# Performance work log

Hardware: AMD Instinct MI355X
Metric: run time of the kernel (lower is better)

## Reference

```python
import jax, jax.numpy as jnp
import numpy as np

B, T, D = 4, 1024, 1024
H, DH = 16, 64
FFN = 4096
CAPACITY = 0.25
C_VAR = 1.0
BETA_CE = 1.0
BETA_CU = 1.0
EPS = 1e-6


def _rmsnorm(x, w, eps=EPS):
    v = jnp.mean(jnp.square(x), axis=-1, keepdims=True)
    return x * jax.lax.rsqrt(v + eps) * w


def _rope(x, pos):
    # x: [B, S, H, DH], pos: [B, S] float positions
    half = x.shape[-1] // 2
    inv = 1.0 / (10000.0 ** (jnp.arange(half, dtype=jnp.float32) / half))
    ang = pos[:, :, None] * inv                      # [B, S, half]
    cos = jnp.cos(ang)[:, :, None, :]                # [B, S, 1, half]
    sin = jnp.sin(ang)[:, :, None, :]
    x1, x2 = x[..., :half], x[..., half:]
    return jnp.concatenate([x1 * cos - x2 * sin, x2 * cos + x1 * sin], axis=-1)


def _decoder(x, pos, ln1, wq, wk, wv, wo, ln2, wg, wu, wd):
    # Qwen2-style decoder layer: RMSNorm -> rotary causal MHA -> res -> RMSNorm -> SwiGLU -> res
    b, s, d = x.shape
    h = _rmsnorm(x, ln1)
    q = _rope((h @ wq).reshape(b, s, H, DH), pos)
    k = _rope((h @ wk).reshape(b, s, H, DH), pos)
    v = (h @ wv).reshape(b, s, H, DH)
    scores = jnp.einsum('bqhd,bkhd->bhqk', q, k) / jnp.sqrt(jnp.float32(DH))
    causal = jnp.tril(jnp.ones((s, s), dtype=bool))
    scores = jnp.where(causal, scores, jnp.finfo(scores.dtype).min)
    attn = jax.nn.softmax(scores, axis=-1)
    o = jnp.einsum('bhqk,bkhd->bqhd', attn, v).reshape(b, s, d) @ wo
    x = x + o
    h2 = _rmsnorm(x, ln2)
    return x + (jax.nn.silu(h2 @ wg) * (h2 @ wu)) @ wd


def _forward(hidden_states, ln1_1, wq1, wk1, wv1, wo1, ln2_1, wg1, wu1, wd1,
             ln1_2, wq2, wk2, wv2, wo2, ln2_2, wg2, wu2, wd2,
             prior_norm_w, prior_w):
    b, t, d = hidden_states.shape
    pos = jnp.broadcast_to(jnp.arange(t, dtype=jnp.float32)[None, :], (b, t))
    # decision layer: full-sequence decoder block
    processed = _decoder(hidden_states, pos, ln1_1, wq1, wk1, wv1, wo1, ln2_1, wg1, wu1, wd1)
    res = processed - hidden_states                  # actual_residual
    # prior network: RMSNorm + linear -> (mu_q, log_var_q)
    prior_h = _rmsnorm(hidden_states, prior_norm_w)
    mu_logvar = prior_h @ prior_w                    # [B, T, 2D]
    mu, logvar = mu_logvar[..., :d], mu_logvar[..., d:]
    # surprise router signals
    d_st = jnp.mean(jnp.square(res), axis=-1)        # [B, T]
    d_ch = jnp.mean(0.5 * (logvar - jnp.log(C_VAR)
                           + (C_VAR + jnp.square(res - mu)) * jnp.exp(-logvar) - 1.0), axis=-1)
    g = jax.nn.sigmoid(BETA_CE * (d_st - jnp.mean(d_st)) + BETA_CU * (d_ch - jnp.mean(d_ch)))
    # top-k selection, sorted by token index (as in the torch code)
    k_sel = max(1, int(t * CAPACITY))
    scores, idx = jax.lax.top_k(g, k_sel)            # [B, k]
    order = jnp.argsort(idx, axis=-1)
    idx = jnp.take_along_axis(idx, order, axis=-1)
    scores = jnp.take_along_axis(scores, order, axis=-1)
    # gather -> decoder layer on selected tokens -> soft-gated scatter back
    bidx = jnp.arange(b)[:, None]
    sel = processed[bidx, idx]                       # [B, k, D]
    y = _decoder(sel, idx.astype(jnp.float32), ln1_2, wq2, wk2, wv2, wo2, ln2_2, wg2, wu2, wd2)
    upd = sel + scores[..., None] * (y - sel)        # soft gating of the block residual
    return processed.at[bidx, idx].set(upd)


def setup_inputs():
    key = jax.random.key(0)
    ks = jax.random.split(key, 16)
    s = 0.02

    def w(k, shape):
        return jax.random.normal(k, shape, dtype=jnp.float32) * s

    inp = {'hidden_states': jax.random.normal(ks[0], (B, T, D), dtype=jnp.float32)}
    for i, n in enumerate(['wq1', 'wk1', 'wv1', 'wo1', 'wq2', 'wk2', 'wv2', 'wo2']):
        inp[n] = w(ks[1 + i], (D, D))
    inp['wg1'] = w(ks[9], (D, FFN)); inp['wu1'] = w(ks[10], (D, FFN)); inp['wd1'] = w(ks[11], (FFN, D))
    inp['wg2'] = w(ks[12], (D, FFN)); inp['wu2'] = w(ks[13], (D, FFN)); inp['wd2'] = w(ks[14], (FFN, D))
    for n in ['ln1_1', 'ln2_1', 'ln1_2', 'ln2_2', 'prior_norm_w']:
        inp[n] = jnp.ones((D,), dtype=jnp.float32)
    inp['prior_w'] = w(ks[15], (D, 2 * D))
    return inp


def reference(hidden_states, ln1_1, wq1, wk1, wv1, wo1, ln2_1, wg1, wu1, wd1,
              ln1_2, wq2, wk2, wv2, wo2, ln2_2, wg2, wu2, wd2,
              prior_norm_w, prior_w):
    return _forward(hidden_states, ln1_1, wq1, wk1, wv1, wo1, ln2_1, wg1, wu1, wd1,
                    ln1_2, wq2, wk2, wv2, wo2, ln2_2, wg2, wu2, wd2,
                    prior_norm_w, prior_w)
```

## Files before the change

### kernel.cpp

```cpp
#include <hip/hip_runtime.h>
#include <math.h>

#define Bdim 4
#define Tdim 1024
#define Ddim 1024
#define Hdim 16
#define DHdim 64
#define FFNdim 4096
#define KSEL 256
#define EPSf 1e-6f

typedef __attribute__((ext_vector_type(8))) short bf16x8;
typedef __attribute__((ext_vector_type(4))) float f32x4;
typedef __attribute__((ext_vector_type(4))) unsigned int u32x4;
typedef unsigned short ushort_t;

#define MFMA_BF16(a,b,c) __builtin_amdgcn_mfma_f32_16x16x32_bf16(a,b,c,0,0,0)

__device__ __forceinline__ int clamp_row(int r){ return r < 0 ? 0 : (r > Tdim-1 ? Tdim-1 : r); }

__device__ __forceinline__ void split8(const float* xs, u32x4* hi, u32x4* lo){
  unsigned int hm[8], lm[8];
  #pragma unroll
  for (int i=0;i<8;i++){
    unsigned int b = __float_as_uint(xs[i]);
    hm[i] = b & 0xFFFF0000u;
    lm[i] = __float_as_uint(xs[i] - __uint_as_float(hm[i]));
  }
  u32x4 h, l;
  #pragma unroll
  for (int i=0;i<4;i++){
    h[i] = (hm[2*i] >> 16) | hm[2*i+1];
    l[i] = (lm[2*i] >> 16) | (lm[2*i+1] & 0xFFFF0000u);
  }
  *hi = h; *lo = l;
}

__device__ __forceinline__ void split1(float x, unsigned int* h16, unsigned int* l16){
  unsigned int b = __float_as_uint(x);
  unsigned int hm = b & 0xFFFF0000u;
  *h16 = hm >> 16;
  *l16 = __float_as_uint(x - __uint_as_float(hm)) >> 16;
}

__global__ void k_fallback(const float* __restrict__ in, float* __restrict__ out, int n){
  int i = blockIdx.x*blockDim.x + threadIdx.x;
  if (i < n) out[i] = in[i];
}

__global__ void k_init_sel(int* __restrict__ selidx, float* __restrict__ selsc, int n){
  int i = blockIdx.x*blockDim.x + threadIdx.x;
  if (i < n){ selidx[i] = i & (KSEL-1); selsc[i] = 0.f; }
}

__global__ __launch_bounds__(256) void k_rmsnorm(const float* __restrict__ x, const float* __restrict__ w,
                          float* __restrict__ y){
  int tok = blockIdx.x;
  const float* xp = x + (size_t)tok*Ddim;
  float* yp = y + (size_t)tok*Ddim;
  int tid = threadIdx.x;
  float s = 0.f;
  float xv[4];
  #pragma unroll
  for (int u = 0; u < 4; u++){ xv[u] = xp[tid + 256*u]; s += xv[u]*xv[u]; }
  __shared__ float red[256];
  red[tid]=s; __syncthreads();
  for (int st=128; st>0; st>>=1){ if (tid<st) red[tid]+=red[tid+st]; __syncthreads(); }
  float r = 1.0f/sqrtf(red[0]/(float)Ddim + EPSf);
  #pragma unroll
  for (int u = 0; u < 4; u++) yp[tid + 256*u] = xv[u]*r*w[tid + 256*u];
}

__global__ __launch_bounds__(256) void k_rmsnorm_sp(const float* __restrict__ x, const float* __restrict__ w,
                          ushort_t* __restrict__ yh, ushort_t* __restrict__ yl){
  int tok = blockIdx.x;
  const float* xp = x + (size_t)tok*Ddim;
  size_t ybase = (size_t)tok*Ddim;
  int tid = threadIdx.x;
  float s = 0.f;
  float xv[4];
  #pragma unroll
  for (int u = 0; u < 4; u++){ xv[u] = xp[tid + 256*u]; s += xv[u]*xv[u]; }
  __shared__ float red[256];
  red[tid]=s; __syncthreads();
  for (int st=128; st>0; st>>=1){ if (tid<st) red[tid]+=red[tid+st]; __syncthreads(); }
  float r = 1.0f/sqrtf(red[0]/(float)Ddim + EPSf);
  #pragma unroll
  for (int u = 0; u < 4; u++){
    float yv = xv[u]*r*w[tid + 256*u];
    unsigned int h16,l16; split1(yv,&h16,&l16);
    yh[ybase + tid + 256*u] = (ushort_t)h16;
    yl[ybase + tid + 256*u] = (ushort_t)l16;
  }
}

__global__ void k_rope(float* __restrict__ x, const int* __restrict__ posidx, int S, int n){
  int e = blockIdx.x*blockDim.x + threadIdx.x;
  if (e >= n) return;
  int j = e & 31;
  int q = e >> 9;
  int t = q % S;
  float pos = posidx ? (float)clamp_row(posidx[q]) : (float)t;
  float inv = exp2f(-0.4152410118609203f * (float)j);
  float ang = pos * inv;
  float c = cosf(ang), s = sinf(ang);
  size_t base = ((size_t)(e >> 5)) * 64;
  float x1 = x[base + j], x2 = x[base + 32 + j];
  x[base + j]      = x1*c - x2*s;
  x[base + 32 + j] = x2*c + x1*s;
}

__global__ void k_rope_sp(const float* __restrict__ x, const int* __restrict__ posidx, int S, int n,
                          ushort_t* __restrict__ Xh, ushort_t* __restrict__ Xl){
  int e = blockIdx.x*blockDim.x + threadIdx.x;
  if (e >= n) return;
  int j = e & 31;
  int q = e >> 9;
  int t = q % S;
  float pos = posidx ? (float)clamp_row(posidx[q]) : (float)t;
  float inv = exp2f(-0.4152410118609203f * (float)j);
  float ang = pos * inv;
  float c = cosf(ang), s = sinf(ang);
  size_t base = ((size_t)(e >> 5)) * 64;
  float x1 = x[base + j], x2 = x[base + 32 + j];
  float y1 = x1*c - x2*s;
  float y2 = x2*c + x1*s;
  unsigned int h16,l16;
  split1(y1,&h16,&l16); Xh[base + j] = (ushort_t)h16; Xl[base + j] = (ushort_t)l16;
  split1(y2,&h16,&l16); Xh[base + 32 + j] = (ushort_t)h16; Xl[base + 32 + j] = (ushort_t)l16;
}

__global__ __launch_bounds__(256) void k_split_w(const float* __restrict__ W,
                          ushort_t* __restrict__ Wh, ushort_t* __restrict__ Wl, int K, int N){
  __shared__ float fs[64][65];
  int n0 = blockIdx.x*64, k0 = blockIdx.y*64;
  int tid = threadIdx.x;
  #pragma unroll
  for (int i=0;i<16;i++){
    int idx = tid + 256*i;
    int r = idx >> 6, c = idx & 63;
    fs[r][c] = W[(size_t)(k0 + r)*N + n0 + c];
  }
  __syncthreads();
  int n = tid >> 2, kq = tid & 3;
  unsigned int hw[8], lw[8];
  #pragma unroll
  for (int i=0;i<16;i+=2){
    float v0 = fs[kq*16+i][n], v1 = fs[kq*16+i+1][n];
    unsigned int h0,l0,h1,l1;
    split1(v0,&h0,&l0); split1(v1,&h1,&l1);
    hw[i>>1] = h0 | (h1<<16);
    lw[i>>1] = l0 | (l1<<16);
  }
  size_t base = (size_t)(n0+n)*K + k0 + kq*16;
  u32x4 a = {hw[0],hw[1],hw[2],hw[3]};
  u32x4 b = {hw[4],hw[5],hw[6],hw[7]};
  *(u32x4*)&Wh[base] = a;
  *(u32x4*)&Wh[base+8] = b;
  u32x4 c2 = {lw[0],lw[1],lw[2],lw[3]};
  u32x4 d2 = {lw[4],lw[5],lw[6],lw[7]};
  *(u32x4*)&Wl[base] = c2;
  *(u32x4*)&Wl[base+8] = d2;
}

__global__ __launch_bounds__(256) void k_attn_mfma(const float* __restrict__ q, const float* __restrict__ k,
                       const float* __restrict__ v, float* __restrict__ o, int S){
  __shared__ ushort_t Kh[64*64], Kl[64*64];
  __shared__ ushort_t Vh[64*64], Vl[64*64];
  __shared__ float Pds[4*16*68];
  const int qt = blockIdx.x, h = blockIdx.y, b = blockIdx.z;
  const int q0 = qt*64;
  const int tid = threadIdx.x;
  const int lane = tid & 63;
  const int ln15 = lane & 15, lk = lane >> 4;
  const int wv = tid >> 6;
  const int qbase = wv*16;
  bf16x8 qa_h[2], qa_l[2];
  {
    const float* qp = q + (((size_t)b*S + q0 + qbase + ln15)*Hdim + h)*64 + lk*8;
    #pragma unroll
    for (int ks=0; ks<2; ks++){
      float xs[8];
      #pragma unroll
      for (int i=0;i<8;i++) xs[i] = qp[ks*32 + i];
      u32x4 hi, lo; split8(xs, &hi, &lo);
      qa_h[ks] = *(bf16x8*)&hi;
      qa_l[ks] = *(bf16x8*)&lo;
    }
  }
  float m_i[4], l_i[4];
  f32x4 oacc[4];
  #pragma unroll
  for (int r=0;r<4;r++){ m_i[r] = -3.4e38f; l_i[r] = 0.f; }
  #pragma unroll
  for (int fd=0;fd<4;fd++){ f32x4 z = {0.f,0.f,0.f,0.f}; oacc[fd] = z; }
  float* Pw = Pds + wv*(16*68);
  for (int j0 = 0; j0 <= q0; j0 += 64){
    __syncthreads();
    {
      int row = tid >> 2;
      int s0 = (tid & 3)*2;
      const float* kp = k + (((size_t)b*S + j0 + row)*Hdim + h)*64 + s0*8;
      #pragma unroll
      for (int g=0; g<2; g++){
        int slot = s0 + g;
        float xs[8];
        #pragma unroll
        for (int i=0;i<8;i++) xs[i] = kp[g*8 + i];
        u32x4 hi, lo; split8(xs, &hi, &lo);
        int base = row*64 + ((slot ^ (row&7))*8);
        *(u32x4*)&Kh[base] = hi;
        *(u32x4*)&Kl[base] = lo;
      }
    }
    {
      int j = tid & 31;
      int dbase = (tid >> 5)*8;
      const float* vp0 = v + (((size_t)b*S + j0 + 2*j)*Hdim + h)*64 + dbase;
      const float* vp1 = vp0 + (size_t)Hdim*64;
      float x0[8], x1[8];
      #pragma unroll
      for (int i=0;i<8;i++){ x0[i]=vp0[i]; x1[i]=vp1[i]; }
      unsigned int* VhW = (unsigned int*)Vh;
      unsigned int* VlW = (unsigned int*)Vl;
      #pragma unroll
      for (int i=0;i<8;i++){
        int d = dbase + i;
        unsigned int h0,l0,h1,l1;
        split1(x0[i], &h0, &l0); split1(x1[i], &h1, &l1);
        int off = d*32 + (((j>>2) ^ (d&7))*4) + (j&3);
        VhW[off] = h0 | (h1<<16);
        VlW[off] = l0 | (l1<<16);
      }
    }
    __syncthreads();
    f32x4 sacc[4];
    #pragma unroll
    for (int fj=0;fj<4;fj++){ f32x4 z = {0.f,0.f,0.f,0.f}; sacc[fj] = z; }
    #pragma unroll
    for (int ks=0; ks<2; ks++){
      #pragma unroll
      for (int fj=0;fj<4;fj++){
        int kr = fj*16 + ln15;
        int idx = kr*64 + (((ks*4+lk) ^ (kr&7))*8);
        bf16x8 kb_h = *(const bf16x8*)&Kh[idx];
        bf16x8 kb_l = *(const bf16x8*)&Kl[idx];
        sacc[fj] = MFMA_BF16(qa_h[ks], kb_h, sacc[fj]);
        sacc[fj] = MFMA_BF16(qa_h[ks], kb_l, sacc[fj]);
        sacc[fj] = MFMA_BF16(qa_l[ks], kb_h, sacc[fj]);
      }
    }
    #pragma unroll
    for (int fj=0;fj<4;fj++){
      int key = j0 + fj*16 + ln15;
      #pragma unroll
      for (int r=0;r<4;r++){
        float sv = sacc[fj][r]*0.125f;
        int qrow = q0 + qbase + lk*4 + r;
        sacc[fj][r] = (key > qrow) ? -3.4e38f : sv;
      }
    }
    float p[4][4];
    #pragma unroll
    for (int r=0;r<4;r++){
      float mt = fmaxf(fmaxf(sacc[0][r],sacc[1][r]), fmaxf(sacc[2][r],sacc[3][r]));
      #pragma unroll
      for (int off=1; off<16; off<<=1) mt = fmaxf(mt, __shfl_xor(mt, off));
      float m_new = fmaxf(m_i[r], mt);
      float alpha = expf(m_i[r] - m_new);
      float rs = 0.f;
      #pragma unroll
      for (int fj=0;fj<4;fj++){
        p[fj][r] = expf(sacc[fj][r] - m_new);
        rs += p[fj][r];
      }
      #pragma unroll
      for (int off=1; off<16; off<<=1) rs += __shfl_xor(rs, off);
      l_i[r] = l_i[r]*alpha + rs;
      m_i[r] = m_new;
      #pragma unroll
      for (int fd=0;fd<4;fd++) oacc[fd][r] *= alpha;
    }
    #pragma unroll
    for (int fj=0;fj<4;fj++)
      #pragma unroll
      for (int r=0;r<4;r++)
        Pw[(lk*4+r)*68 + fj*16 + ln15] = p[fj][r];
    #pragma unroll
    for (int ks=0; ks<2; ks++){
      f32x4 pf0 = *(const f32x4*)&Pw[ln15*68 + ks*32 + lk*8];
      f32x4 pf1 = *(const f32x4*)&Pw[ln15*68 + ks*32 + lk*8 + 4];
      float xs[8] = {pf0[0],pf0[1],pf0[2],pf0[3],pf1[0],pf1[1],pf1[2],pf1[3]};
      u32x4 hi, lo; split8(xs, &hi, &lo);
      bf16x8 pa_h = *(bf16x8*)&hi;
      bf16x8 pa_l = *(bf16x8*)&lo;
      #pragma unroll
      for (int fd=0;fd<4;fd++){
        int d = fd*16 + ln15;
        int idx = d*64 + (((ks*4+lk) ^ (d&7))*8);
        bf16x8 vb_h = *(const bf16x8*)&Vh[idx];
        bf16x8 vb_l = *(const bf16x8*)&Vl[idx];
        oacc[fd] = MFMA_BF16(pa_h, vb_h, oacc[fd]);
        oacc[fd] = MFMA_BF16(pa_h, vb_l, oacc[fd]);
        oacc[fd] = MFMA_BF16(pa_l, vb_h, oacc[fd]);
      }
    }
  }
  #pragma unroll
  for (int r=0;r<4;r++){
    float inv_l = 1.0f/l_i[r];
    #pragma unroll
    for (int fd=0;fd<4;fd++){
      o[(((size_t)b*S + q0 + qbase + lk*4 + r)*Hdim + h)*64 + fd*16 + ln15] = oacc[fd][r]*inv_l;
    }
  }
}

__global__ __launch_bounds__(256) void k_attn_ps(
    const ushort_t* __restrict__ Qph, const ushort_t* __restrict__ Qpl,
    const ushort_t* __restrict__ Kph, const ushort_t* __restrict__ Kpl,
    const ushort_t* __restrict__ Vph, const ushort_t* __restrict__ Vpl,
    ushort_t* __restrict__ Oh, ushort_t* __restrict__ Ol, int S){
  __shared__ ushort_t Kh[64*64], Kl[64*64];
  __shared__ ushort_t Vh[64*64], Vl[64*64];
  __shared__ float Pds[4*16*68];
  const int qt = blockIdx.x, h = blockIdx.y, b = blockIdx.z;
  const int q0 = qt*64;
  const int tid = threadIdx.x;
  const int lane = tid & 63;
  const int ln15 = lane & 15, lk = lane >> 4;
  const int wv = tid >> 6;
  const int qbase = wv*16;
  bf16x8 qa_h[2], qa_l[2];
  {
    size_t qoff = (((size_t)b*S + q0 + qbase + ln15)*Hdim + h)*64;
    #pragma unroll
    for (int ks=0; ks<2; ks++){
      qa_h[ks] = *(const bf16x8*)&Qph[qoff + ks*32 + lk*8];
      qa_l[ks] = *(const bf16x8*)&Qpl[qoff + ks*32 + lk*8];
    }
  }
  float m_i[4], lp[4];
  f32x4 oacc[4];
  #pragma unroll
  for (int r=0;r<4;r++){ m_i[r] = -3.4e38f; lp[r] = 0.f; }
  #pragma unroll
  for (int fd=0;fd<4;fd++){ f32x4 z = {0.f,0.f,0.f,0.f}; oacc[fd] = z; }
  float* Pw = Pds + wv*(16*68);
  for (int j0 = 0; j0 <= q0; j0 += 64){
    __syncthreads();
    #pragma unroll
    for (int g=0; g<2; g++){
      int row = g*32 + (tid >> 3);
      int ks = tid & 7;
      size_t ga = (((size_t)b*S + j0 + row)*Hdim + h)*64 + ks*8;
      u32x4 hi = *(const u32x4*)&Kph[ga];
      u32x4 lo = *(const u32x4*)&Kpl[ga];
      int base = row*64 + ((ks ^ (row&7))*8);
      *(u32x4*)&Kh[base] = hi;
      *(u32x4*)&Kl[base] = lo;
    }
    {
      int j = tid & 31;
      int dbase = (tid >> 5)*8;
      size_t g0 = (((size_t)b*S + j0 + 2*j)*Hdim + h)*64 + dbase;
      size_t g1 = g0 + (size_t)Hdim*64;
      u32x4 ah = *(const u32x4*)&Vph[g0];
      u32x4 bh = *(const u32x4*)&Vph[g1];
      u32x4 al = *(const u32x4*)&Vpl[g0];
      u32x4 bl = *(const u32x4*)&Vpl[g1];
      unsigned int* VhW = (unsigned int*)Vh;
      unsigned int* VlW = (unsigned int*)Vl;
      #pragma unroll
      for (int i=0;i<4;i++){
        int d0 = dbase + 2*i, d1 = d0 + 1;
        int off0 = d0*32 + (((j>>2) ^ (d0&7))*4) + (j&3);
        int off1 = d1*32 + (((j>>2) ^ (d1&7))*4) + (j&3);
        VhW[off0] = (ah[i] & 0xFFFFu) | (bh[i] << 16);
        VhW[off1] = (ah[i] >> 16)     | (bh[i] & 0xFFFF0000u);
        VlW[off0] = (al[i] & 0xFFFFu) | (bl[i] << 16);
        VlW[off1] = (al[i] >> 16)     | (bl[i] & 0xFFFF0000u);
      }
    }
    __syncthreads();
    f32x4 sacc[4];
    #pragma unroll
    for (int fj=0;fj<4;fj++){ f32x4 z = {0.f,0.f,0.f,0.f}; sacc[fj] = z; }
    #pragma unroll
    for (int ks=0; ks<2; ks++){
      #pragma unroll
      for (int fj=0;fj<4;fj++){
        int kr = fj*16 + ln15;
        int idx = kr*64 + (((ks*4+lk) ^ (kr&7))*8);
        bf16x8 kb_h = *(const bf16x8*)&Kh[idx];
        bf16x8 kb_l = *(const bf16x8*)&Kl[idx];
        sacc[fj] = MFMA_BF16(qa_h[ks], kb_h, sacc[fj]);
        sacc[fj] = MFMA_BF16(qa_h[ks], kb_l, sacc[fj]);
        sacc[fj] = MFMA_BF16(qa_l[ks], kb_h, sacc[fj]);
      }
    }
    #pragma unroll
    for (int fj=0;fj<4;fj++){
      int key = j0 + fj*16 + ln15;
      #pragma unroll
      for (int r=0;r<4;r++){
        float sv = sacc[fj][r]*0.125f;
        int qrow = q0 + qbase + lk*4 + r;
        sacc[fj][r] = (key > qrow) ? -3.4e38f : sv;
      }
    }
    float tm[4];
    #pragma unroll
    for (int r=0;r<4;r++)
      tm[r] = fmaxf(fmaxf(sacc[0][r],sacc[1][r]), fmaxf(sacc[2][r],sacc[3][r]));
    bool okl = (tm[0] <= m_i[0]+8.f) & (tm[1] <= m_i[1]+8.f)
             & (tm[2] <= m_i[2]+8.f) & (tm[3] <= m_i[3]+8.f);
    float p[4][4];
    if (__all(okl)){
      #pragma unroll
      for (int r=0;r<4;r++){
        #pragma unroll
        for (int fj=0;fj<4;fj++){
          float pv = expf(sacc[fj][r] - m_i[r]);
          p[fj][r] = pv;
          lp[r] += pv;
        }
      }
    } else {
      #pragma unroll
      for (int r=0;r<4;r++){
        float mt = tm[r];
        #pragma unroll
        for (int off=1; off<16; off<<=1) mt = fmaxf(mt, __shfl_xor(mt, off));
        float m_new = fmaxf(m_i[r], mt);
        float alpha = expf(m_i[r] - m_new);
        lp[r] *= alpha;
        #pragma unroll
        for (int fd=0;fd<4;fd++) oacc[fd][r] *= alpha;
        m_i[r] = m_new;
        #pragma unroll
        for (int fj=0;fj<4;fj++){
          float pv = expf(sacc[fj][r] - m_new);
          p[fj][r] = pv;
          lp[r] += pv;
        }
      }
    }
    #pragma unroll
    for (int fj=0;fj<4;fj++)
      #pragma unroll
      for (int r=0;r<4;r++)
        Pw[(lk*4+r)*68 + fj*16 + ln15] = p[fj][r];
    #pragma unroll
    for (int ks=0; ks<2; ks++){
      f32x4 pf0 = *(const f32x4*)&Pw[ln15*68 + ks*32 + lk*8];
      f32x4 pf1 = *(const f32x4*)&Pw[ln15*68 + ks*32 + lk*8 + 4];
      float xs[8] = {pf0[0],pf0[1],pf0[2],pf0[3],pf1[0],pf1[1],pf1[2],pf1[3]};
      u32x4 hi, lo; split8(xs, &hi, &lo);
      bf16x8 pa_h = *(bf16x8*)&hi;
      bf16x8 pa_l = *(bf16x8*)&lo;
      #pragma unroll
      for (int fd=0;fd<4;fd++){
        int d = fd*16 + ln15;
        int idx = d*64 + (((ks*4+lk) ^ (d&7))*8);
        bf16x8 vb_h = *(const bf16x8*)&Vh[idx];
        bf16x8 vb_l = *(const bf16x8*)&Vl[idx];
        oacc[fd] = MFMA_BF16(pa_h, vb_h, oacc[fd]);
        oacc[fd] = MFMA_BF16(pa_h, vb_l, oacc[fd]);
        oacc[fd] = MFMA_BF16(pa_l, vb_h, oacc[fd]);
      }
    }
  }
  #pragma unroll
  for (int r=0;r<4;r++){
    float l = lp[r];
    #pragma unroll
    for (int off=1; off<16; off<<=1) l += __shfl_xor(l, off);
    float inv_l = 1.0f/l;
    #pragma unroll
    for (int fd=0;fd<4;fd++){
      float val = oacc[fd][r]*inv_l;
      unsigned int h16,l16; split1(val,&h16,&l16);
      size_t cix = (((size_t)b*S + q0 + qbase + lk*4 + r)*Hdim + h)*64 + fd*16 + ln15;
      Oh[cix] = (ushort_t)h16;
      Ol[cix] = (ushort_t)l16;
    }
  }
}

__global__ __launch_bounds__(256) void k_gemm_mfma(
    const float* __restrict__ A, const float* __restrict__ W,
    float* __restrict__ C, const float* __restrict__ addv,
    int K, int ldw, int ldc){
  __shared__ ushort_t Ah[128*32], Al[128*32], Bh[128*32], Bl[128*32];
  const int tid = threadIdx.x;
  const int row0 = blockIdx.y*128, col0 = blockIdx.x*128;
  const int lane = tid & 63;
  const int ln15 = lane & 15, lk = lane >> 4;
  const int wv = tid >> 6;
  const int wrow0 = (wv >> 1)*64, wcol0 = (wv & 1)*64;
  const int arow = tid >> 2;
  const int aks  = tid & 3;
  const int bcol = tid & 127;
  const int bks0 = tid >> 7;
  f32x4 acc[4][4];
  #pragma unroll
  for (int i=0;i<4;i++)
    #pragma unroll
    for (int j=0;j<4;j++){ f32x4 z = {0.f,0.f,0.f,0.f}; acc[i][j] = z; }
  for (int k0 = 0; k0 < K; k0 += 32){
    #pragma unroll
    for (int g=0; g<2; g++){
      int row = g*64 + arow;
      const float* ap = A + (size_t)(row0+row)*K + k0 + aks*8;
      float xs[8];
      #pragma unroll
      for (int i=0;i<8;i++) xs[i] = ap[i];
      u32x4 hi, lo; split8(xs, &hi, &lo);
      int base = row*32 + ((aks ^ ((row>>1)&3))*8);
      *(u32x4*)&Ah[base] = hi;
      *(u32x4*)&Al[base] = lo;
    }
    #pragma unroll
    for (int g=0; g<2; g++){
      int ks = bks0 + 2*g;
      const float* wp = W + (size_t)(k0 + ks*8)*ldw + col0 + bcol;
      float xs[8];
      #pragma unroll
      for (int i=0;i<8;i++) xs[i] = wp[(size_t)i*ldw];
      u32x4 hi, lo; split8(xs, &hi, &lo);
      int base = bcol*32 + ((ks ^ ((bcol>>1)&3))*8);
      *(u32x4*)&Bh[base] = hi;
      *(u32x4*)&Bl[base] = lo;
    }
    __syncthreads();
    bf16x8 ah[4], al[4];
    #pragma unroll
    for (int fi=0;fi<4;fi++){
      int r = wrow0 + fi*16 + ln15;
      int idx = r*32 + ((lk ^ ((r>>1)&3))*8);
      ah[fi] = *(const bf16x8*)&Ah[idx];
      al[fi] = *(const bf16x8*)&Al[idx];
    }
    #pragma unroll
    for (int fj=0;fj<4;fj++){
      int c = wcol0 + fj*16 + ln15;
      int idx = c*32 + ((lk ^ ((c>>1)&3))*8);
      bf16x8 bh = *(const bf16x8*)&Bh[idx];
      bf16x8 bl = *(const bf16x8*)&Bl[idx];
      #pragma unroll
      for (int fi=0;fi<4;fi++){
        acc[fi][fj] = MFMA_BF16(ah[fi], bh, acc[fi][fj]);
        acc[fi][fj] = MFMA_BF16(ah[fi], bl, acc[fi][fj]);
        acc[fi][fj] = MFMA_BF16(al[fi], bh, acc[fi][fj]);
      }
    }
    __syncthreads();
  }
  #pragma unroll
  for (int fi=0;fi<4;fi++){
    #pragma unroll
    for (int fj=0;fj<4;fj++){
      f32x4 v = acc[fi][fj];
      int cc = col0 + wcol0 + fj*16 + ln15;
      #pragma unroll
      for (int r=0;r<4;r++){
        size_t cix = (size_t)(row0 + wrow0 + fi*16 + lk*4 + r)*ldc + cc;
        float val = v[r];
        if (addv) val += addv[cix];
        C[cix] = val;
      }
    }
  }
}

__global__ __launch_bounds__(512) void k_gemm_ps(
    const ushort_t* __restrict__ Ahp, const ushort_t* __restrict__ Alp, int lda,
    const ushort_t* __restrict__ Bhp, const ushort_t* __restrict__ Blp, int ldb,
    float* __restrict__ C, ushort_t* __restrict__ Chp, ushort_t* __restrict__ Clp,
    const float* __restrict__ addv, int K, int ldc){
  __shared__ ushort_t Ah[128*32], Al[128*32], Bh[128*32], Bl[128*32];
  const int tid = threadIdx.x;
  const int row0 = blockIdx.y*128, col0 = blockIdx.x*128;
  const int lane = tid & 63;
  const int ln15 = lane & 15, lk = lane >> 4;
  const int wv = tid >> 6;
  const int wrow0 = (wv >> 2)*64, wcol0 = (wv & 3)*32;
  const int t8 = tid >> 2, ks4 = tid & 3;
  const int sbase = t8*32 + ((ks4 ^ ((t8>>1)&3))*8);
  const size_t gaBase = (size_t)(row0 + t8)*lda + ks4*8;
  const size_t gbBase = (size_t)(col0 + t8)*ldb + ks4*8;

  f32x4 acc[4][2];
  #pragma unroll
  for (int i=0;i<4;i++)
    #pragma unroll
    for (int j=0;j<2;j++){ f32x4 z = {0.f,0.f,0.f,0.f}; acc[i][j] = z; }

  u32x4 rAh = *(const u32x4*)&Ahp[gaBase];
  u32x4 rAl = *(const u32x4*)&Alp[gaBase];
  u32x4 rBh = *(const u32x4*)&Bhp[gbBase];
  u32x4 rBl = *(const u32x4*)&Blp[gbBase];

  for (int k0 = 0; k0 < K; k0 += 32){
    __syncthreads();
    *(u32x4*)&Ah[sbase] = rAh;
    *(u32x4*)&Al[sbase] = rAl;
    *(u32x4*)&Bh[sbase] = rBh;
    *(u32x4*)&Bl[sbase] = rBl;
    __syncthreads();
    if (k0 + 32 < K){
      rAh = *(const u32x4*)&Ahp[gaBase + k0 + 32];
      rAl = *(const u32x4*)&Alp[gaBase + k0 + 32];
      rBh = *(const u32x4*)&Bhp[gbBase + k0 + 32];
      rBl = *(const u32x4*)&Blp[gbBase + k0 + 32];
    }
    bf16x8 ah[4], al[4];
    #pragma unroll
    for (int fi=0;fi<4;fi++){
      int r = wrow0 + fi*16 + ln15;
      int idx = r*32 + ((lk ^ ((r>>1)&3))*8);
      ah[fi] = *(const bf16x8*)&Ah[idx];
      al[fi] = *(const bf16x8*)&Al[idx];
    }
    #pragma unroll
// ... 370 lines not shown
  const float* xp = x0 + (size_t)tok*Ddim;
  const float* mu = muB + (size_t)tok*Ddim;
  const float* lv = lvB + (size_t)tok*Ddim;
  float s1=0.f, s2=0.f;
  for (int i=tid;i<Ddim;i+=256){
    float r = pp[i]-xp[i];
    s1 += r*r;
    float t = r - mu[i];
    float l = lv[i];
    s2 += 0.5f*(l + (1.0f + t*t)*expf(-l) - 1.0f);
  }
  __shared__ float red[256], red2[256];
  red[tid]=s1; red2[tid]=s2; __syncthreads();
  for (int st=128; st>0; st>>=1){ if (tid<st){red[tid]+=red[tid+st]; red2[tid]+=red2[tid+st];} __syncthreads(); }
  if (tid==0){ dst[tok]=red[0]/(float)Ddim; dch[tok]=red2[0]/(float)Ddim; }
}

__global__ __launch_bounds__(1024) void k_gate(const float* __restrict__ dst, const float* __restrict__ dch,
                        float* __restrict__ g){
  int tid = threadIdx.x;
  float s1=0.f, s2=0.f;
  for (int i=tid; i<Bdim*Tdim; i+=1024){ s1+=dst[i]; s2+=dch[i]; }
  __shared__ float r1[1024], r2[1024];
  r1[tid]=s1; r2[tid]=s2; __syncthreads();
  for (int st=512; st>0; st>>=1){ if(tid<st){r1[tid]+=r1[tid+st]; r2[tid]+=r2[tid+st];} __syncthreads(); }
  float m1 = r1[0]/(float)(Bdim*Tdim), m2 = r2[0]/(float)(Bdim*Tdim);
  for (int i=tid; i<Bdim*Tdim; i+=1024){
    float z = (dst[i]-m1) + (dch[i]-m2);
    g[i] = 1.0f/(1.0f+expf(-z));
  }
}

__global__ __launch_bounds__(1024) void k_select(const float* __restrict__ g, int* __restrict__ selidx,
                         float* __restrict__ selsc){
  int b = blockIdx.x, t = threadIdx.x;
  __shared__ float gs[1024];
  __shared__ int flag[1024];
  float gv = g[b*Tdim + t];
  if (!(gv == gv)) gv = -3.4e38f;
  gs[t] = gv; __syncthreads();
  float gi = gs[t];
  int rank = 0;
  for (int j=0;j<Tdim;j++){
    float gj = gs[j];
    rank += (gj > gi) || (gj == gi && j < t);
  }
  int sel = (rank < KSEL) ? 1 : 0;
  flag[t] = sel; __syncthreads();
  if (sel){
    int pos = 0;
    for (int j=0;j<t;j++) pos += flag[j];
    if (pos < KSEL){
      selidx[b*KSEL+pos] = t;
      selsc[b*KSEL+pos] = gi;
    }
  }
}

__global__ __launch_bounds__(256) void k_gather(const float* __restrict__ proc, const int* __restrict__ selidx,
                         float* __restrict__ sel){
  int j = blockIdx.x, b = blockIdx.y, tid = threadIdx.x;
  int row = clamp_row(selidx[b*KSEL+j]);
  const float* src = proc + ((size_t)b*Tdim + row)*Ddim;
  float* dst = sel + ((size_t)b*KSEL + j)*Ddim;
  for (int d=tid; d<Ddim; d+=256) dst[d]=src[d];
}

__global__ void k_out(const float* __restrict__ proc, float* __restrict__ out, int n){
  int i = blockIdx.x*blockDim.x + threadIdx.x;
  if (i<n) out[i] = proc[i];
}

__global__ __launch_bounds__(256) void k_scatter(const float* __restrict__ sel, const float* __restrict__ y,
                          const float* __restrict__ selsc, const int* __restrict__ selidx,
                          float* __restrict__ out){
  int j = blockIdx.x, b = blockIdx.y, tid = threadIdx.x;
  int row = clamp_row(selidx[b*KSEL+j]);
  float s = selsc[b*KSEL+j];
  const float* sp = sel + ((size_t)b*KSEL + j)*Ddim;
  const float* yp = y + ((size_t)b*KSEL + j)*Ddim;
  float* op = out + ((size_t)b*Tdim + row)*Ddim;
  for (int d=tid; d<Ddim; d+=256){
    op[d] = sp[d] + s*(yp[d]-sp[d]);
  }
}

extern "C" void kernel_launch(void* const* d_in, const int* in_sizes, int n_in,
                              void* d_out, int out_size, void* d_ws, size_t ws_size,
                              hipStream_t stream){
  (void)in_sizes; (void)n_in; (void)out_size;
  const float* hidden = (const float*)d_in[0];
  const float* wq1 = (const float*)d_in[1];
  const float* wk1 = (const float*)d_in[2];
  const float* wv1 = (const float*)d_in[3];
  const float* wo1 = (const float*)d_in[4];
  const float* wq2 = (const float*)d_in[5];
  const float* wk2 = (const float*)d_in[6];
  const float* wv2 = (const float*)d_in[7];
  const float* wo2 = (const float*)d_in[8];
  const float* wg1 = (const float*)d_in[9];
  const float* wu1 = (const float*)d_in[10];
  const float* wd1 = (const float*)d_in[11];
  const float* wg2 = (const float*)d_in[12];
  const float* wu2 = (const float*)d_in[13];
  const float* wd2 = (const float*)d_in[14];
  const float* ln1_1 = (const float*)d_in[15];
  const float* ln2_1 = (const float*)d_in[16];
  const float* ln1_2 = (const float*)d_in[17];
  const float* ln2_2 = (const float*)d_in[18];
  const float* prior_norm = (const float*)d_in[19];
  const float* prior_w = (const float*)d_in[20];

  const size_t A = (size_t)Bdim*Tdim*Ddim;
  const size_t Q = (size_t)Bdim*KSEL*Ddim;
  const int n = (int)A;
  const int MT = Bdim*Tdim;
  const int M2 = Bdim*KSEL;

  const size_t WELEMS = 34u*1024*1024;
  size_t need_old = (4*A + 16384) * sizeof(float);
  size_t need_new = need_old + 2*WELEMS*sizeof(ushort_t);

  if (ws_size < need_old){
    k_fallback<<<(n+255)/256,256,0,stream>>>(hidden, (float*)d_out, n);
    return;
  }

  float* ws = (float*)d_ws;
  float* R0 = ws;
  float* R1 = ws + 1*A;
  float* R2 = ws + 2*A;
  float* R3 = ws + 3*A;
  float* dstb = ws + 4*A;
  float* dchb = dstb + 4096;
  float* gb   = dchb + 4096;
  float* selsc= gb + 4096;
  int*   selidx = (int*)(selsc + 1024);

  k_init_sel<<<4,256,0,stream>>>(selidx, selsc, Bdim*KSEL);

  if (ws_size >= need_new){
    ushort_t* wpb = (ushort_t*)(ws + 4*A + 16384);
    size_t cur = 0;
    const size_t M1x1 = (size_t)1024*1024;
    const size_t M1x4 = (size_t)1024*4096;
    #define ALLOCW(nm, KN) ushort_t* nm##_h = wpb + cur; ushort_t* nm##_l = wpb + cur + (KN); cur += 2*(size_t)(KN);
    ALLOCW(pwq1, M1x1) ALLOCW(pwk1, M1x1) ALLOCW(pwv1, M1x1) ALLOCW(pwo1, M1x1)
    ALLOCW(pwq2, M1x1) ALLOCW(pwk2, M1x1) ALLOCW(pwv2, M1x1) ALLOCW(pwo2, M1x1)
    ALLOCW(pwg1, M1x4) ALLOCW(pwu1, M1x4) ALLOCW(pwd1, M1x4)
    ALLOCW(pwg2, M1x4) ALLOCW(pwu2, M1x4) ALLOCW(pwd2, M1x4)
    ALLOCW(ppw, (size_t)2048*1024)
    #undef ALLOCW

    k_split_w<<<dim3(16,16),256,0,stream>>>(wq1, pwq1_h, pwq1_l, 1024, 1024);
    k_split_w<<<dim3(16,16),256,0,stream>>>(wk1, pwk1_h, pwk1_l, 1024, 1024);
    k_split_w<<<dim3(16,16),256,0,stream>>>(wv1, pwv1_h, pwv1_l, 1024, 1024);
    k_split_w<<<dim3(16,16),256,0,stream>>>(wo1, pwo1_h, pwo1_l, 1024, 1024);
    k_split_w<<<dim3(16,16),256,0,stream>>>(wq2, pwq2_h, pwq2_l, 1024, 1024);
    k_split_w<<<dim3(16,16),256,0,stream>>>(wk2, pwk2_h, pwk2_l, 1024, 1024);
    k_split_w<<<dim3(16,16),256,0,stream>>>(wv2, pwv2_h, pwv2_l, 1024, 1024);
    k_split_w<<<dim3(16,16),256,0,stream>>>(wo2, pwo2_h, pwo2_l, 1024, 1024);
    k_split_w<<<dim3(64,16),256,0,stream>>>(wg1, pwg1_h, pwg1_l, 1024, 4096);
    k_split_w<<<dim3(64,16),256,0,stream>>>(wu1, pwu1_h, pwu1_l, 1024, 4096);
    k_split_w<<<dim3(16,64),256,0,stream>>>(wd1, pwd1_h, pwd1_l, 4096, 1024);
    k_split_w<<<dim3(64,16),256,0,stream>>>(wg2, pwg2_h, pwg2_l, 1024, 4096);
    k_split_w<<<dim3(64,16),256,0,stream>>>(wu2, pwu2_h, pwu2_l, 1024, 4096);
    k_split_w<<<dim3(16,64),256,0,stream>>>(wd2, pwd2_h, pwd2_l, 4096, 1024);
    k_split_w<<<dim3(32,16),256,0,stream>>>(prior_w, ppw_h, ppw_l, 1024, 2048);

    ushort_t* Hh = (ushort_t*)R0; ushort_t* Hl = Hh + A;
    k_rmsnorm_sp<<<MT,256,0,stream>>>(hidden, ln1_1, Hh, Hl);
    ushort_t* Vp_h = (ushort_t*)R3; ushort_t* Vp_l = Vp_h + A;
    k_gemm_qkv<<<dim3(8, MT/128, 3),512,0,stream>>>(Hh,Hl,1024,
        pwq1_h,pwq1_l, pwk1_h,pwk1_l, pwv1_h,pwv1_l, 1024,
        R1, R2, Vp_h, Vp_l, 1024, 1024);
    int nr = MT*Hdim*32;
    ushort_t* Qp_h = (ushort_t*)R0; ushort_t* Qp_l = Qp_h + A;
    k_rope_sp<<<(nr+255)/256,256,0,stream>>>(R1, nullptr, Tdim, nr, Qp_h, Qp_l);
    ushort_t* Kp_h = (ushort_t*)R1; ushort_t* Kp_l = Kp_h + A;
    k_rope_sp<<<(nr+255)/256,256,0,stream>>>(R2, nullptr, Tdim, nr, Kp_h, Kp_l);
    ushort_t* Op_h = (ushort_t*)R2; ushort_t* Op_l = Op_h + A;
    k_attn_ps<<<dim3(Tdim/64,Hdim,Bdim),256,0,stream>>>(Qp_h,Qp_l, Kp_h,Kp_l, Vp_h,Vp_l, Op_h,Op_l, Tdim);
    k_gemm_ps<<<dim3(8, MT/128),512,0,stream>>>(Op_h,Op_l,1024, pwo1_h,pwo1_l,1024, R1, nullptr,nullptr, hidden, 1024, 1024);
    ushort_t* H2h = (ushort_t*)R0; ushort_t* H2l = H2h + A;
    k_rmsnorm_sp<<<MT,256,0,stream>>>(R1, ln2_1, H2h, H2l);
    ushort_t* ACTh = (ushort_t*)R3; ushort_t* ACTl = ACTh + A;
    for (int c = 0; c < 4; c++){
      k_gemm_dual_ps<<<dim3(16, MT/128),512,0,stream>>>(H2h,H2l,1024,
          pwg1_h + (size_t)c*M1x1, pwg1_l + (size_t)c*M1x1,
          pwu1_h + (size_t)c*M1x1, pwu1_l + (size_t)c*M1x1, 1024,
          ACTh, ACTl, 1024, 1024);
      k_gemm_ps<<<dim3(8, MT/128),512,0,stream>>>(ACTh,ACTl,1024,
          pwd1_h + (size_t)c*1024, pwd1_l + (size_t)c*1024, 4096,
          R2, nullptr,nullptr, (c==0 ? R1 : R2), 1024, 1024);
    }

    ushort_t* PHh = (ushort_t*)R0; ushort_t* PHl = PHh + A;
    k_rmsnorm_sp<<<MT,256,0,stream>>>(hidden, prior_norm, PHh, PHl);
    k_gemm_qkv<<<dim3(8, MT/128, 2),512,0,stream>>>(PHh,PHl,1024,
        ppw_h,ppw_l, ppw_h + M1x1, ppw_l + M1x1, nullptr,nullptr, 1024,
        R1, R3, nullptr,nullptr, 1024, 1024);
    k_dstch2<<<MT,256,0,stream>>>(R2, hidden, R1, R3, dstb, dchb);
    k_gate<<<1,1024,0,stream>>>(dstb, dchb, gb);
    k_select<<<Bdim,1024,0,stream>>>(gb, selidx, selsc);
    float* SELX = R0;
    k_gather<<<dim3(KSEL,Bdim),256,0,stream>>>(R2, selidx, SELX);

    ushort_t* h2h = (ushort_t*)R1;        ushort_t* h2l = h2h + Q;
    k_rmsnorm_sp<<<M2,256,0,stream>>>(SELX, ln1_2, h2h, h2l);
    float* q2f = R1 + Q;
    float* k2f = R1 + 2*Q;
    ushort_t* v2h = (ushort_t*)(R1 + 3*Q); ushort_t* v2l = v2h + Q;
    k_gemm_qkv<<<dim3(8, M2/128, 3),512,0,stream>>>(h2h,h2l,1024,
        pwq2_h,pwq2_l, pwk2_h,pwk2_l, pwv2_h,pwv2_l, 1024,
        q2f, k2f, v2h, v2l, 1024, 1024);
    int nr2 = M2*Hdim*32;
    ushort_t* q2ph = (ushort_t*)(R0 + Q);   ushort_t* q2pl = q2ph + Q;
    ushort_t* k2ph = (ushort_t*)(R0 + 2*Q); ushort_t* k2pl = k2ph + Q;
    k_rope_sp<<<(nr2+255)/256,256,0,stream>>>(q2f, selidx, KSEL, nr2, q2ph, q2pl);
    k_rope_sp<<<(nr2+255)/256,256,0,stream>>>(k2f, selidx, KSEL, nr2, k2ph, k2pl);
    ushort_t* o2h = (ushort_t*)(R0 + 3*Q);  ushort_t* o2l = o2h + Q;
    k_attn_ps<<<dim3(KSEL/64,Hdim,Bdim),256,0,stream>>>(q2ph,q2pl, k2ph,k2pl, v2h,v2l, o2h,o2l, KSEL);
    float* X12 = R1 + Q;
    k_gemm_ps<<<dim3(8, M2/128),512,0,stream>>>(o2h,o2l,1024, pwo2_h,pwo2_l,1024, X12, nullptr,nullptr, SELX, 1024, 1024);
    ushort_t* h22h = (ushort_t*)(R1 + 2*Q); ushort_t* h22l = h22h + Q;
    k_rmsnorm_sp<<<M2,256,0,stream>>>(X12, ln2_2, h22h, h22l);
    ushort_t* act2h = (ushort_t*)(R1 + 3*Q); ushort_t* act2l = act2h + Q;
    float* Y = R3;
    for (int c = 0; c < 4; c++){
      k_gemm_dual_ps<<<dim3(16, M2/128),512,0,stream>>>(h22h,h22l,1024,
          pwg2_h + (size_t)c*M1x1, pwg2_l + (size_t)c*M1x1,
          pwu2_h + (size_t)c*M1x1, pwu2_l + (size_t)c*M1x1, 1024,
          act2h, act2l, 1024, 1024);
      k_gemm_ps<<<dim3(8, M2/128),512,0,stream>>>(act2h,act2l,1024,
          pwd2_h + (size_t)c*1024, pwd2_l + (size_t)c*1024, 4096,
          Y, nullptr,nullptr, (c==0 ? X12 : Y), 1024, 1024);
    }
    k_out<<<(n+255)/256,256,0,stream>>>(R2, (float*)d_out, n);
    k_scatter<<<dim3(KSEL,Bdim),256,0,stream>>>(SELX, Y, selsc, selidx, (float*)d_out);
    return;
  }

  k_rmsnorm<<<MT,256,0,stream>>>(hidden, ln1_1, R0);
  dim3 gD(Ddim/128, MT/128);
  k_gemm_mfma<<<gD,256,0,stream>>>(R0, wq1, R1, nullptr, Ddim, Ddim, Ddim);
  k_gemm_mfma<<<gD,256,0,stream>>>(R0, wk1, R2, nullptr, Ddim, Ddim, Ddim);
  k_gemm_mfma<<<gD,256,0,stream>>>(R0, wv1, R3, nullptr, Ddim, Ddim, Ddim);
  int nr = MT*Hdim*32;
  k_rope<<<(nr+255)/256,256,0,stream>>>(R1, nullptr, Tdim, nr);
  k_rope<<<(nr+255)/256,256,0,stream>>>(R2, nullptr, Tdim, nr);
  k_attn_mfma<<<dim3(Tdim/64,Hdim,Bdim),256,0,stream>>>(R1, R2, R3, R0, Tdim);
  k_gemm_mfma<<<gD,256,0,stream>>>(R0, wo1, R1, hidden, Ddim, Ddim, Ddim);
  k_rmsnorm<<<MT,256,0,stream>>>(R1, ln2_1, R2);
  for (int c = 0; c < 4; c++){
    k_gemm_dual_mfma<<<dim3(1024/64, MT/128),256,0,stream>>>(R2, wg1 + (size_t)c*1024, wu1 + (size_t)c*1024,
                                                  R3, Ddim, FFNdim, 1024);
    k_gemm_mfma<<<dim3(Ddim/128, MT/128),256,0,stream>>>(R3, wd1 + (size_t)c*1024*Ddim, R0,
                                             (c==0 ? R1 : R0), 1024, Ddim, Ddim);
  }
  k_rmsnorm<<<MT,256,0,stream>>>(hidden, prior_norm, R1);
  k_gemm_mfma<<<dim3(2*Ddim/128, MT/128),256,0,stream>>>(R1, prior_w, R2, nullptr, Ddim, 2*Ddim, 2*Ddim);
  k_dstch<<<MT,256,0,stream>>>(R0, hidden, R2, dstb, dchb);
  k_gate<<<1,1024,0,stream>>>(dstb, dchb, gb);
  k_select<<<Bdim,1024,0,stream>>>(gb, selidx, selsc);
  k_gather<<<dim3(KSEL,Bdim),256,0,stream>>>(R0, selidx, R1);
  k_rmsnorm<<<M2,256,0,stream>>>(R1, ln1_2, R2);
  dim3 gD2(Ddim/128, M2/128);
  k_gemm_mfma<<<gD2,256,0,stream>>>(R2, wq2, R2+Q,   nullptr, Ddim, Ddim, Ddim);
  k_gemm_mfma<<<gD2,256,0,stream>>>(R2, wk2, R2+2*Q, nullptr, Ddim, Ddim, Ddim);
  k_gemm_mfma<<<gD2,256,0,stream>>>(R2, wv2, R2+3*Q, nullptr, Ddim, Ddim, Ddim);
  int nr2 = M2*Hdim*32;
  k_rope<<<(nr2+255)/256,256,0,stream>>>(R2+Q,   nullptr, KSEL, nr2);
  k_rope<<<(nr2+255)/256,256,0,stream>>>(R2+2*Q, nullptr, KSEL, nr2);
  k_rope<<<(nr2+255)/256,256,0,stream>>>(R2+Q,   selidx, KSEL, 0);
  k_attn_mfma<<<dim3(KSEL/64,Hdim,Bdim),256,0,stream>>>(R2+Q, R2+2*Q, R2+3*Q, R3, KSEL);
  k_gemm_mfma<<<gD2,256,0,stream>>>(R3, wo2, R3+Q, R1, Ddim, Ddim, Ddim);
  k_rmsnorm<<<M2,256,0,stream>>>(R3+Q, ln2_2, R3+2*Q);
  for (int c = 0; c < 4; c++){
    k_gemm_dual_mfma<<<dim3(1024/64, M2/128),256,0,stream>>>(R3+2*Q, wg2 + (size_t)c*1024, wu2 + (size_t)c*1024,
                                                  R3+3*Q, Ddim, FFNdim, 1024);
    k_gemm_mfma<<<dim3(Ddim/128, M2/128),256,0,stream>>>(R3+3*Q, wd2 + (size_t)c*1024*Ddim, R2,
                                             (c==0 ? R3+Q : R2), 1024, Ddim, Ddim);
  }
  k_out<<<(n+255)/256,256,0,stream>>>(R0, (float*)d_out, n);
  k_scatter<<<dim3(KSEL,Bdim),256,0,stream>>>(R1, R2, selsc, selidx, (float*)d_out);
}
```

Measured before the change: 1.379 ms.

## Prefetch KV tiles in attention, batch weight splits, reverse tile order, fix rope positions

The causal attention kernel now loads the next K/V tile from global memory into registers while the current tile is being computed, so load latency overlaps with MFMA work. Query tiles are visited in reverse order so the longest causal blocks are scheduled first, which should balance the tail of the grid. The many per-weight hi/lo split launches are merged into three batched launches indexed by blockIdx.z, cutting launch overhead. The second-layer rope calls are changed to use the selected indices for both Q and K, which alters behaviour on that path. The prefetch costs extra registers per thread.

New measurement: 1.420 ms. 3.0% more time.

```diff
diff --git a/kernel.cpp b/kernel.cpp
--- a/kernel.cpp
+++ b/kernel.cpp
@@ -130,6 +130,46 @@
   split1(y2,&h16,&l16); Xh[base + 32 + j] = (ushort_t)h16; Xl[base + 32 + j] = (ushort_t)l16;
 }
 
+struct SplitJobs {
+  const float* W[8];
+  ushort_t* Wh[8];
+  ushort_t* Wl[8];
+};
+__global__ __launch_bounds__(256) void k_split_wz(SplitJobs jobs, int K, int N){
+  const float* W = jobs.W[blockIdx.z];
+  ushort_t* Wh = jobs.Wh[blockIdx.z];
+  ushort_t* Wl = jobs.Wl[blockIdx.z];
+  __shared__ float fs[64][65];
+  int n0 = blockIdx.x*64, k0 = blockIdx.y*64;
+  int tid = threadIdx.x;
+  #pragma unroll
+  for (int i=0;i<16;i++){
+    int idx = tid + 256*i;
+    int r = idx >> 6, c = idx & 63;
+    fs[r][c] = W[(size_t)(k0 + r)*N + n0 + c];
+  }
+  __syncthreads();
+  int n = tid >> 2, kq = tid & 3;
+  unsigned int hw[8], lw[8];
+  #pragma unroll
+  for (int i=0;i<16;i+=2){
+    float v0 = fs[kq*16+i][n], v1 = fs[kq*16+i+1][n];
+    unsigned int h0,l0,h1,l1;
+    split1(v0,&h0,&l0); split1(v1,&h1,&l1);
+    hw[i>>1] = h0 | (h1<<16);
+    lw[i>>1] = l0 | (l1<<16);
+  }
+  size_t base = (size_t)(n0+n)*K + k0 + kq*16;
+  u32x4 a = {hw[0],hw[1],hw[2],hw[3]};
+  u32x4 b = {hw[4],hw[5],hw[6],hw[7]};
+  *(u32x4*)&Wh[base] = a;
+  *(u32x4*)&Wh[base+8] = b;
+  u32x4 c2 = {lw[0],lw[1],lw[2],lw[3]};
+  u32x4 d2 = {lw[4],lw[5],lw[6],lw[7]};
+  *(u32x4*)&Wl[base] = c2;
+  *(u32x4*)&Wl[base+8] = d2;
+}
+
 __global__ __launch_bounds__(256) void k_split_w(const float* __restrict__ W,
                           ushort_t* __restrict__ Wh, ushort_t* __restrict__ Wl, int K, int N){
   __shared__ float fs[64][65];
@@ -324,7 +364,8 @@
   __shared__ ushort_t Kh[64*64], Kl[64*64];
   __shared__ ushort_t Vh[64*64], Vl[64*64];
   __shared__ float Pds[4*16*68];
-  const int qt = blockIdx.x, h = blockIdx.y, b = blockIdx.z;
+  const int qt = (gridDim.x - 1) - blockIdx.x;
+  const int h = blockIdx.y, b = blockIdx.z;
   const int q0 = qt*64;
   const int tid = threadIdx.x;
   const int lane = tid & 63;
@@ -340,6 +381,19 @@
       qa_l[ks] = *(const bf16x8*)&Qpl[qoff + ks*32 + lk*8];
     }
   }
+  const int krow = tid >> 3, kks = tid & 7;
+  const int vj = tid & 31, vdbase = (tid >> 5)*8;
+  u32x4 rKh[2], rKl[2], rVah, rVbh, rVal, rVbl;
+  #define LOAD_KV(J0) { \
+    size_t ga0 = (((size_t)b*S + (J0) + krow)*Hdim + h)*64 + kks*8; \
+    size_t ga1 = (((size_t)b*S + (J0) + 32 + krow)*Hdim + h)*64 + kks*8; \
+    rKh[0] = *(const u32x4*)&Kph[ga0]; rKl[0] = *(const u32x4*)&Kpl[ga0]; \
+    rKh[1] = *(const u32x4*)&Kph[ga1]; rKl[1] = *(const u32x4*)&Kpl[ga1]; \
+    size_t g0 = (((size_t)b*S + (J0) + 2*vj)*Hdim + h)*64 + vdbase; \
+    size_t g1 = g0 + (size_t)Hdim*64; \
+    rVah = *(const u32x4*)&Vph[g0]; rVbh = *(const u32x4*)&Vph[g1]; \
+    rVal = *(const u32x4*)&Vpl[g0]; rVbl = *(const u32x4*)&Vpl[g1]; }
+
   float m_i[4], lp[4];
   f32x4 oacc[4];
   #pragma unroll
@@ -347,42 +401,33 @@
   #pragma unroll
   for (int fd=0;fd<4;fd++){ f32x4 z = {0.f,0.f,0.f,0.f}; oacc[fd] = z; }
   float* Pw = Pds + wv*(16*68);
+
+  LOAD_KV(0);
   for (int j0 = 0; j0 <= q0; j0 += 64){
     __syncthreads();
     #pragma unroll
     for (int g=0; g<2; g++){
-      int row = g*32 + (tid >> 3);
-      int ks = tid & 7;
-      size_t ga = (((size_t)b*S + j0 + row)*Hdim + h)*64 + ks*8;
-      u32x4 hi = *(const u32x4*)&Kph[ga];
-      u32x4 lo = *(const u32x4*)&Kpl[ga];
-      int base = row*64 + ((ks ^ (row&7))*8);
-      *(u32x4*)&Kh[base] = hi;
-      *(u32x4*)&Kl[base] = lo;
+      int row = g*32 + krow;
+      int base = row*64 + ((kks ^ (row&7))*8);
+      *(u32x4*)&Kh[base] = rKh[g];
+      *(u32x4*)&Kl[base] = rKl[g];
     }
     {
-      int j = tid & 31;
-      int dbase = (tid >> 5)*8;
-      size_t g0 = (((size_t)b*S + j0 + 2*j)*Hdim + h)*64 + dbase;
-      size_t g1 = g0 + (size_t)Hdim*64;
-      u32x4 ah = *(const u32x4*)&Vph[g0];
-      u32x4 bh = *(const u32x4*)&Vph[g1];
-      u32x4 al = *(const u32x4*)&Vpl[g0];
-      u32x4 bl = *(const u32x4*)&Vpl[g1];
       unsigned int* VhW = (unsigned int*)Vh;
       unsigned int* VlW = (unsigned int*)Vl;
       #pragma unroll
       for (int i=0;i<4;i++){
-        int d0 = dbase + 2*i, d1 = d0 + 1;
-        int off0 = d0*32 + (((j>>2) ^ (d0&7))*4) + (j&3);
-        int off1 = d1*32 + (((j>>2) ^ (d1&7))*4) + (j&3);
-        VhW[off0] = (ah[i] & 0xFFFFu) | (bh[i] << 16);
-        VhW[off1] = (ah[i] >> 16)     | (bh[i] & 0xFFFF0000u);
-        VlW[off0] = (al[i] & 0xFFFFu) | (bl[i] << 16);
-        VlW[off1] = (al[i] >> 16)     | (bl[i] & 0xFFFF0000u);
+        int d0 = vdbase + 2*i, d1 = d0 + 1;
+        int off0 = d0*32 + (((vj>>2) ^ (d0&7))*4) + (vj&3);
+        int off1 = d1*32 + (((vj>>2) ^ (d1&7))*4) + (vj&3);
+        VhW[off0] = (rVah[i] & 0xFFFFu) | (rVbh[i] << 16);
+        VhW[off1] = (rVah[i] >> 16)     | (rVbh[i] & 0xFFFF0000u);
+        VlW[off0] = (rVal[i] & 0xFFFFu) | (rVbl[i] << 16);
+        VlW[off1] = (rVal[i] >> 16)     | (rVbl[i] & 0xFFFF0000u);
       }
     }
     __syncthreads();
+    if (j0 + 64 <= q0){ LOAD_KV(j0 + 64); }
     f32x4 sacc[4];
     #pragma unroll
     for (int fj=0;fj<4;fj++){ f32x4 z = {0.f,0.f,0.f,0.f}; sacc[fj] = z; }
@@ -471,6 +516,7 @@
       }
     }
   }
+  #undef LOAD_KV
   #pragma unroll
   for (int r=0;r<4;r++){
     float l = lp[r];
@@ -1147,21 +1193,31 @@
     ALLOCW(ppw, (size_t)2048*1024)
     #undef ALLOCW
 
-    k_split_w<<<dim3(16,16),256,0,stream>>>(wq1, pwq1_h, pwq1_l, 1024, 1024);
-    k_split_w<<<dim3(16,16),256,0,stream>>>(wk1, pwk1_h, pwk1_l, 1024, 1024);
-    k_split_w<<<dim3(16,16),256,0,stream>>>(wv1, pwv1_h, pwv1_l, 1024, 1024);
-    k_split_w<<<dim3(16,16),256,0,stream>>>(wo1, pwo1_h, pwo1_l, 1024, 1024);
-    k_split_w<<<dim3(16,16),256,0,stream>>>(wq2, pwq2_h, pwq2_l, 1024, 1024);
-    k_split_w<<<dim3(16,16),256,0,stream>>>(wk2, pwk2_h, pwk2_l, 1024, 1024);
-    k_split_w<<<dim3(16,16),256,0,stream>>>(wv2, pwv2_h, pwv2_l, 1024, 1024);
-    k_split_w<<<dim3(16,16),256,0,stream>>>(wo2, pwo2_h, pwo2_l, 1024, 1024);
-    k_split_w<<<dim3(64,16),256,0,stream>>>(wg1, pwg1_h, pwg1_l, 1024, 4096);
-    k_split_w<<<dim3(64,16),256,0,stream>>>(wu1, pwu1_h, pwu1_l, 1024, 4096);
-    k_split_w<<<dim3(16,64),256,0,stream>>>(wd1, pwd1_h, pwd1_l, 4096, 1024);
-    k_split_w<<<dim3(64,16),256,0,stream>>>(wg2, pwg2_h, pwg2_l, 1024, 4096);
-    k_split_w<<<dim3(64,16),256,0,stream>>>(wu2, pwu2_h, pwu2_l, 1024, 4096);
-    k_split_w<<<dim3(16,64),256,0,stream>>>(wd2, pwd2_h, pwd2_l, 4096, 1024);
-    k_split_w<<<dim3(32,16),256,0,stream>>>(prior_w, ppw_h, ppw_l, 1024, 2048);
+    {
+      SplitJobs sq;
+      sq.W[0]=wq1; sq.Wh[0]=pwq1_h; sq.Wl[0]=pwq1_l;
+      sq.W[1]=wk1; sq.Wh[1]=pwk1_h; sq.Wl[1]=pwk1_l;
+      sq.W[2]=wv1; sq.Wh[2]=pwv1_h; sq.Wl[2]=pwv1_l;
+      sq.W[3]=wo1; sq.Wh[3]=pwo1_h; sq.Wl[3]=pwo1_l;
+      sq.W[4]=wq2; sq.Wh[4]=pwq2_h; sq.Wl[4]=pwq2_l;
+      sq.W[5]=wk2; sq.Wh[5]=pwk2_h; sq.Wl[5]=pwk2_l;
+      sq.W[6]=wv2; sq.Wh[6]=pwv2_h; sq.Wl[6]=pwv2_l;
+      sq.W[7]=wo2; sq.Wh[7]=pwo2_h; sq.Wl[7]=pwo2_l;
+      k_split_wz<<<dim3(16,16,8),256,0,stream>>>(sq, 1024, 1024);
+      SplitJobs gu;
+      gu.W[0]=wg1; gu.Wh[0]=pwg1_h; gu.Wl[0]=pwg1_l;
+      gu.W[1]=wu1; gu.Wh[1]=pwu1_h; gu.Wl[1]=pwu1_l;
+      gu.W[2]=wg2; gu.Wh[2]=pwg2_h; gu.Wl[2]=pwg2_l;
+      gu.W[3]=wu2; gu.Wh[3]=pwu2_h; gu.Wl[3]=pwu2_l;
+      for (int i=4;i<8;i++){ gu.W[i]=wg1; gu.Wh[i]=pwg1_h; gu.Wl[i]=pwg1_l; }
+      k_split_wz<<<dim3(64,16,4),256,0,stream>>>(gu, 1024, 4096);
+      SplitJobs wd;
+      wd.W[0]=wd1; wd.Wh[0]=pwd1_h; wd.Wl[0]=pwd1_l;
+      wd.W[1]=wd2; wd.Wh[1]=pwd2_h; wd.Wl[1]=pwd2_l;
+      for (int i=2;i<8;i++){ wd.W[i]=wd1; wd.Wh[i]=pwd1_h; wd.Wl[i]=pwd1_l; }
+      k_split_wz<<<dim3(16,64,2),256,0,stream>>>(wd, 4096, 1024);
+      k_split_w<<<dim3(32,16),256,0,stream>>>(prior_w, ppw_h, ppw_l, 1024, 2048);
+    }
 
     ushort_t* Hh = (ushort_t*)R0; ushort_t* Hl = Hh + A;
     k_rmsnorm_sp<<<MT,256,0,stream>>>(hidden, ln1_1, Hh, Hl);
@@ -1265,9 +1321,8 @@
   k_gemm_mfma<<<gD2,256,0,stream>>>(R2, wk2, R2+2*Q, nullptr, Ddim, Ddim, Ddim);
   k_gemm_mfma<<<gD2,256,0,stream>>>(R2, wv2, R2+3*Q, nullptr, Ddim, Ddim, Ddim);
   int nr2 = M2*Hdim*32;
-  k_rope<<<(nr2+255)/256,256,0,stream>>>(R2+Q,   nullptr, KSEL, nr2);
-  k_rope<<<(nr2+255)/256,256,0,stream>>>(R2+2*Q, nullptr, KSEL, nr2);
-  k_rope<<<(nr2+255)/256,256,0,stream>>>(R2+Q,   selidx, KSEL, 0);
+  k_rope<<<(nr2+255)/256,256,0,stream>>>(R2+Q,   selidx, KSEL, nr2);
+  k_rope<<<(nr2+255)/256,256,0,stream>>>(R2+2*Q, selidx, KSEL, nr2);
   k_attn_mfma<<<dim3(KSEL/64,Hdim,Bdim),256,0,stream>>>(R2+Q, R2+2*Q, R2+3*Q, R3, KSEL);
   k_gemm_mfma<<<gD2,256,0,stream>>>(R3, wo2, R3+Q, R1, Ddim, Ddim, Ddim);
   k_rmsnorm<<<M2,256,0,stream>>>(R3+Q, ln2_2, R3+2*Q);
```
